# Kernel optimization log

Hardware: AMD Instinct MI355X
Metric: run time of the kernel (lower is better)

Reference implementation:

```python
import jax, jax.numpy as jnp
import numpy as np

N = 50000      # nodes
E = 800000     # edges (avg degree 16)
H = 4          # heads
C = 64         # per-head dim (= hidden_dim, TransformerConv out_channels)
D = H * C      # 256, concat output dim
VOCAB = 100


def setup_inputs() -> dict:
    key = jax.random.key(0)
    ks = jax.random.split(key, 16)
    f = lambda k, shape: (jax.random.normal(k, shape, jnp.float32) * 0.05)
    return {
        "x": jax.random.randint(ks[0], (N,), 0, VOCAB),
        "edge_index": jax.random.randint(ks[1], (2, E), 0, N),
        "embed": f(ks[2], (VOCAB, C)),        # node_embed table (hidden_dim=64)
        "Wq": f(ks[3], (C, D)), "bq": f(ks[4], (D,)),
        "Wk": f(ks[5], (C, D)), "bk": f(ks[6], (D,)),
        "Wv": f(ks[7], (C, D)), "bv": f(ks[8], (D,)),
        "Wskip": f(ks[9], (C, D)), "bskip": f(ks[10], (D,)),
        "Wbeta": f(ks[11], (3 * D, 1)),       # lin_beta has no bias in PyG
        "Wcoop": f(ks[12], (D, 1)), "bcoop": f(ks[13], (1,)),
        "Wanom": f(ks[14], (D, 1)), "banom": f(ks[15], (1,)),
    }


def _segment_softmax(logits, seg, num_segments):
    # logits: [E, H], seg: [E] destination-node ids
    m = jax.ops.segment_max(logits, seg, num_segments=num_segments)   # [N, H]
    ex = jnp.exp(logits - m[seg])
    s = jax.ops.segment_sum(ex, seg, num_segments=num_segments)       # [N, H]
    return ex / (s[seg] + 1e-16)


def _transformer_conv(h, src, dst, Wq, bq, Wk, bk, Wv, bv, Wskip, bskip, Wbeta):
    # h: [N, C] node features; src->dst edges; PyG TransformerConv(beta=True)
    q = (h @ Wq + bq).reshape(N, H, C)
    k = (h @ Wk + bk).reshape(N, H, C)
    v = (h @ Wv + bv).reshape(N, H, C)
    # per-edge attention logits: query of dst, key of src
    logits = (q[dst] * k[src]).sum(-1) / np.sqrt(C)    # [E, H]
    alpha = _segment_softmax(logits, dst, N)           # softmax over in-edges of dst
    msg = v[src] * alpha[..., None]                    # [E, H, C]
    out = jax.ops.segment_sum(msg, dst, num_segments=N).reshape(N, D)
    # beta-gated skip connection
    x_r = h @ Wskip + bskip                            # [N, D]
    beta = jax.nn.sigmoid(jnp.concatenate([out, x_r, out - x_r], axis=-1) @ Wbeta)
    return beta * x_r + (1.0 - beta) * out             # [N, D]


def reference(x, edge_index, embed, Wq, bq, Wk, bk, Wv, bv,
              Wskip, bskip, Wbeta, Wcoop, bcoop, Wanom, banom):
    h = embed[x]                                       # long input -> embedding
    src, dst = edge_index[0], edge_index[1]
    h = _transformer_conv(h, src, dst, Wq, bq, Wk, bk, Wv, bv, Wskip, bskip, Wbeta)
    h = jax.nn.relu(h)                                 # dropout is identity (eval)
    cooperation = jax.nn.sigmoid(h @ Wcoop + bcoop)    # [N, 1]
    anomaly = jax.nn.sigmoid(h @ Wanom + banom)        # [N, 1]
    return cooperation, anomaly, h
```

## Files before the change

### kernel.cpp

```cpp
#include <hip/hip_runtime.h>
#include <hip/hip_bf16.h>
#include <hip/hip_fp16.h>

typedef __hip_bfloat16 bf16;

#define NN 50000
#define EE 800000
#define VOCABSZ 100
#define DD 256
#define NW 25
#define MAXD 64
#define NBUCK 500
#define BNODES 100
#define AWG 500
#define EPW 1600
#define PCAP 24

static __device__ __forceinline__ float b2f(bf16 v) { return __bfloat162float(v); }

static __device__ __forceinline__ float ldf(const void* p, int i, int isf32) {
  if (isf32) return ((const float*)p)[i];
  return b2f(((const bf16*)p)[i]);
}

static __device__ __forceinline__ int block_detect(const unsigned short* e16) {
  __shared__ int f;
  if (threadIdx.x == 0) f = 0;
  __syncthreads();
  unsigned int ex = (e16[threadIdx.x] >> 7) & 0xFF;
  unsigned long long any = __ballot(ex >= 128);
  if ((threadIdx.x & 63) == 0 && any) atomicOr(&f, 1);
  __syncthreads();
  return f;
}

__global__ __launch_bounds__(256) void k_phase1(
    const void* __restrict__ embed,
    const void* __restrict__ Wq, const void* __restrict__ bq,
    const void* __restrict__ Wk, const void* __restrict__ bk,
    const void* __restrict__ Wv, const void* __restrict__ bv,
    const void* __restrict__ Ws, const void* __restrict__ bs,
    const void* __restrict__ Wbeta,
    const void* __restrict__ Wcoop, const void* __restrict__ bcoop,
    const void* __restrict__ Wanom, const void* __restrict__ banom,
    float* __restrict__ Qt, float* __restrict__ Kt,
    __half* __restrict__ VtH, __half* __restrict__ StH,
    float* __restrict__ Wf, int* __restrict__ flag,
    const int4* __restrict__ src4, const int4* __restrict__ dst4,
    const int* __restrict__ x,
    unsigned char* __restrict__ cnt, unsigned short* __restrict__ seg)
{
  __shared__ float e[64];
  __shared__ unsigned int cur[NBUCK];
  const int t = threadIdx.x;
  const unsigned bx = blockIdx.x;

  if (bx >= 500) {
    const unsigned w = bx - 500;
    for (int i = t; i < NBUCK; i += 256) cur[i] = 0;
    __syncthreads();
    const int g0 = w * (EPW / 4);
    for (int g = t; g < EPW / 4; g += 256) {
      int4 s = src4[g0 + g];
      int4 d = dst4[g0 + g];
      int xv0 = x[s.x], xv1 = x[s.y], xv2 = x[s.z], xv3 = x[s.w];
      unsigned b0 = (unsigned)d.x / BNODES, b1 = (unsigned)d.y / BNODES;
      unsigned b2 = (unsigned)d.z / BNODES, b3 = (unsigned)d.w / BNODES;
      unsigned p0 = atomicAdd(&cur[b0], 1u);
      unsigned p1 = atomicAdd(&cur[b1], 1u);
      unsigned p2 = atomicAdd(&cur[b2], 1u);
      unsigned p3 = atomicAdd(&cur[b3], 1u);
      if (p0 < PCAP) seg[((size_t)b0 * AWG + w) * PCAP + p0] =
          (unsigned short)(((unsigned)d.x - b0 * BNODES) | ((unsigned)xv0 << 7));
      if (p1 < PCAP) seg[((size_t)b1 * AWG + w) * PCAP + p1] =
          (unsigned short)(((unsigned)d.y - b1 * BNODES) | ((unsigned)xv1 << 7));
      if (p2 < PCAP) seg[((size_t)b2 * AWG + w) * PCAP + p2] =
          (unsigned short)(((unsigned)d.z - b2 * BNODES) | ((unsigned)xv2 << 7));
      if (p3 < PCAP) seg[((size_t)b3 * AWG + w) * PCAP + p3] =
          (unsigned short)(((unsigned)d.w - b3 * BNODES) | ((unsigned)xv3 << 7));
    }
    __syncthreads();
    for (int i = t; i < NBUCK; i += 256) {
      unsigned c = cur[i]; if (c > PCAP) c = PCAP;
      cnt[(size_t)i * AWG + w] = (unsigned char)c;
    }
    return;
  }

  const int y = bx / 100;
  const int row = bx % 100;
  if (y == 4 && row != 0) return;

  int isf32 = block_detect((const unsigned short*)embed);

  if (y == 4) {
    Wf[t]       = ldf(Wbeta, t, isf32)       + ldf(Wbeta, 512 + t, isf32);
    Wf[256 + t] = ldf(Wbeta, 256 + t, isf32) - ldf(Wbeta, 512 + t, isf32);
    Wf[512 + t] = ldf(Wcoop, t, isf32);
    Wf[768 + t] = ldf(Wanom, t, isf32);
    if (t == 0) {
      Wf[1024] = ldf(bcoop, 0, isf32);
      Wf[1025] = ldf(banom, 0, isf32);
      flag[0] = isf32;
    }
    return;
  }

  if (t < 64) e[t] = ldf(embed, row * 64 + t, isf32);
  __syncthreads();
  const void* W; const void* b;
  switch (y) {
    case 0:  W = Wq; b = bq; break;
    case 1:  W = Wk; b = bk; break;
    case 2:  W = Wv; b = bv; break;
    default: W = Ws; b = bs; break;
  }
  float acc;
  if (isf32) {
    const float* w32 = (const float*)W;
    acc = ((const float*)b)[t];
    #pragma unroll 8
    for (int c = 0; c < 64; ++c) acc = fmaf(e[c], w32[c * DD + t], acc);
  } else {
    const bf16* w16 = (const bf16*)W;
    acc = b2f(((const bf16*)b)[t]);
    #pragma unroll 8
    for (int c = 0; c < 64; ++c) acc = fmaf(e[c], b2f(w16[c * DD + t]), acc);
  }
  switch (y) {
    case 0:  Qt[row * DD + t] = acc; break;
    case 1:  Kt[row * DD + t] = acc; break;
    case 2:  VtH[row * DD + t] = __float2half(acc); break;
    default: StH[row * DD + t] = __float2half(acc); break;
  }
}

__global__ __launch_bounds__(256) void k_phase2(
    const float* __restrict__ Qt, const float* __restrict__ Kt,
    float* __restrict__ Et,
    const unsigned char* __restrict__ cnt, const unsigned short* __restrict__ seg,
    int* __restrict__ deg, unsigned short* __restrict__ ell16)
{
  __shared__ float q[DD];
  __shared__ unsigned int hist[BNODES * NW];
  const int t = threadIdx.x;
  const unsigned bx = blockIdx.x;

  if (bx < 100) {
    const int a = bx;
    q[t] = Qt[a * DD + t];
    __syncthreads();
    for (int idx = t; idx < VOCABSZ * 4; idx += 256) {
      int b = idx >> 2, h = idx & 3;
      const float* kk = Kt + b * DD + h * 64;
      const float* qq = q + h * 64;
      float acc = 0.f;
      #pragma unroll 8
      for (int c = 0; c < 64; ++c) acc += qq[c] * kk[c];
      Et[(a * VOCABSZ + b) * 4 + h] = __expf(acc * 0.125f);
    }
    return;
  }

  const int b = bx - 100;
  for (int i = t; i < BNODES * NW; i += 256) hist[i] = 0;
  __syncthreads();
  for (int w = t; w < AWG; w += 256) {
    const size_t sbase = (size_t)b * AWG + w;
    int c = (int)cnt[sbase];
    if (!c) continue;
    const uint4* sp4 = (const uint4*)(seg + sbase * PCAP);
    uint4 q0 = sp4[0];
    uint4 q1 = make_uint4(0u, 0u, 0u, 0u);
    uint4 q2 = make_uint4(0u, 0u, 0u, 0u);
    if (c > 8)  q1 = sp4[1];
    if (c > 16) q2 = sp4[2];
    unsigned wd[12] = { q0.x, q0.y, q0.z, q0.w, q1.x, q1.y, q1.z, q1.w,
                        q2.x, q2.y, q2.z, q2.w };
    #pragma unroll
    for (int i = 0; i < 12; ++i) {
      unsigned lo = wd[i] & 0xFFFFu;
      unsigned hi = wd[i] >> 16;
      if (2 * i < c)
        atomicAdd(&hist[(lo & 127u) * NW + ((lo >> 7) >> 2)], 1u << (((lo >> 7) & 3) * 8));
      if (2 * i + 1 < c)
        atomicAdd(&hist[(hi & 127u) * NW + ((hi >> 7) >> 2)], 1u << (((hi >> 7) & 3) * 8));
    }
  }
  __syncthreads();
  if (t < BNODES) {
    int n = b * BNODES + t;
    const unsigned int* cw = hist + t * NW;
    unsigned short* dp = ell16 + (size_t)n * MAXD;
    int k = 0;
    #pragma unroll
    for (int w = 0; w < NW; ++w) {
      unsigned word = cw[w];
      if (!word) continue;
      #pragma unroll
      for (int bb = 0; bb < 4; ++bb) {
        unsigned c = (word >> (8 * bb)) & 255u;
        if (c) { if (k < MAXD) dp[k] = (unsigned short)((unsigned)(w * 4 + bb) | (c << 8)); k++; }
      }
    }
    deg[n] = (k < MAXD) ? k : MAXD;
  }
}

__global__ __launch_bounds__(256) void k_node(
    const int* __restrict__ x, const int* __restrict__ deg,
    const unsigned short* __restrict__ ell16,
    const __half* __restrict__ VtH, const __half* __restrict__ StH,
    const float* __restrict__ Et, const float* __restrict__ Wf,
    void* __restrict__ out, const int* __restrict__ flag)
{
  __shared__ uint2 evs[4][2][32][4];
  const int t = threadIdx.x;
  const int lane = t & 63;
  const int wv = t >> 6;
  const int l31 = lane & 31;
  const int half = lane >> 5;
  const int hbase = lane & 32;
  const int n = blockIdx.x * 8 + wv * 2 + half;
  const int cb = l31 << 3;
  const int head = l31 >> 3;

  const int xd = x[n];
  const int dgn = deg[n];
  const int dgA = __shfl(dgn, 0, 64);
  const int dgB = __shfl(dgn, 32, 64);
  const int dmax = max(dgA, dgB);

  unsigned int mye = (l31 < dgn) ? (unsigned int)ell16[(size_t)n * MAXD + l31] : 0u;
  const int myxs = (int)(mye & 255u);
  const float mycnt = (float)(mye >> 8);
  const unsigned rowoff = (unsigned)myxs << 9;

  float4 ev = *reinterpret_cast<const float4*>(Et + xd * (VOCABSZ * 4) + myxs * 4);
  ev.x *= mycnt; ev.y *= mycnt; ev.z *= mycnt; ev.w *= mycnt;
  uint4* evp = reinterpret_cast<uint4*>(&evs[wv][half][l31][0]);
  evp[0] = make_uint4(__float_as_uint(ev.x), rowoff, __float_as_uint(ev.y), rowoff);
  evp[1] = make_uint4(__float_as_uint(ev.z), rowoff, __float_as_uint(ev.w), rowoff);

  union HF8U { uint4 u; __half2 h2[4]; };
  HF8U xru; xru.u = *reinterpret_cast<const uint4*>(StH + xd * DD + cb);
  const float4 wo0 = *reinterpret_cast<const float4*>(Wf + cb);
  const float4 wo1 = *reinterpret_cast<const float4*>(Wf + cb + 4);
  const float4 wx0 = *reinterpret_cast<const float4*>(Wf + 256 + cb);
  const float4 wx1 = *reinterpret_cast<const float4*>(Wf + 256 + cb + 4);

  const uint2* __restrict__ myev = &evs[wv][half][0][head];
  const char* __restrict__ vbase = reinterpret_cast<const char*>(VtH) + (cb << 1);

  float s = 0.f;
  __half2 a0 = __float2half2_rn(0.f), a1 = __float2half2_rn(0.f);
  __half2 a2 = __float2half2_rn(0.f), a3 = __float2half2_rn(0.f);

  const int j1 = (dmax < 32) ? dmax : 32;
  #pragma unroll 4
  for (int j = 0; j < j1; ++j) {
    uint2 ue = myev[j * 4];
    float e = __uint_as_float(ue.x);
    s += e;
    __half2 e2 = __float2half2_rn(e);
    HF8U vv; vv.u = *reinterpret_cast<const uint4*>(vbase + ue.y);
    a0 = __hfma2(e2, vv.h2[0], a0);
    a1 = __hfma2(e2, vv.h2[1], a1);
    a2 = __hfma2(e2, vv.h2[2], a2);
    a3 = __hfma2(e2, vv.h2[3], a3);
  }
  if (dmax > 32) {
    const float* __restrict__ Erow = Et + xd * (VOCABSZ * 4) + head;
    unsigned int mye2 = (l31 + 32 < dgn) ? (unsigned int)ell16[(size_t)n * MAXD + 32 + l31] : 0u;
    for (int j = 32; j < dmax; ++j) {
      unsigned int en = (unsigned int)__shfl((int)mye2, hbase + (j - 32), 64);
      int xs = (int)(en & 255u);
      float e = (float)(en >> 8) * Erow[xs << 2];
      s += e;
      __half2 e2 = __float2half2_rn(e);
      HF8U vv; vv.u = *reinterpret_cast<const uint4*>(vbase + ((unsigned)xs << 9));
      a0 = __hfma2(e2, vv.h2[0], a0);
      a1 = __hfma2(e2, vv.h2[1], a1);
      a2 = __hfma2(e2, vv.h2[2], a2);
      a3 = __hfma2(e2, vv.h2[3], a3);
    }
  }

  const float inv = 1.f / (s + 1e-16f);
  float o[8] = { __low2float(a0)*inv, __high2float(a0)*inv,
                 __low2float(a1)*inv, __high2float(a1)*inv,
                 __low2float(a2)*inv, __high2float(a2)*inv,
                 __low2float(a3)*inv, __high2float(a3)*inv };
  float xr[8] = { __low2float(xru.h2[0]), __high2float(xru.h2[0]),
                  __low2float(xru.h2[1]), __high2float(xru.h2[1]),
                  __low2float(xru.h2[2]), __high2float(xru.h2[2]),
                  __low2float(xru.h2[3]), __high2float(xru.h2[3]) };

  float bp = o[0]*wo0.x + o[1]*wo0.y + o[2]*wo0.z + o[3]*wo0.w
           + o[4]*wo1.x + o[5]*wo1.y + o[6]*wo1.z + o[7]*wo1.w
           + xr[0]*wx0.x + xr[1]*wx0.y + xr[2]*wx0.z + xr[3]*wx0.w
           + xr[4]*wx1.x + xr[5]*wx1.y + xr[6]*wx1.z + xr[7]*wx1.w;
  #pragma unroll
  for (int m = 16; m >= 1; m >>= 1) bp += __shfl_xor(bp, m, 64);
  const float beta = 1.f / (1.f + __expf(-bp));

  const float4 wc0 = *reinterpret_cast<const float4*>(Wf + 512 + cb);
  const float4 wc1 = *reinterpret_cast<const float4*>(Wf + 512 + cb + 4);
  const float4 wa0 = *reinterpret_cast<const float4*>(Wf + 768 + cb);
  const float4 wa1 = *reinterpret_cast<const float4*>(Wf + 768 + cb + 4);
  const float wcv[8] = { wc0.x, wc0.y, wc0.z, wc0.w, wc1.x, wc1.y, wc1.z, wc1.w };
  const float wav[8] = { wa0.x, wa0.y, wa0.z, wa0.w, wa1.x, wa1.y, wa1.z, wa1.w };

  float h[8];
  float pc = 0.f, pa = 0.f;
  #pragma unroll
  for (int j = 0; j < 8; ++j) {
    float hv = beta * xr[j] + (1.f - beta) * o[j];
    hv = fmaxf(hv, 0.f);
    h[j] = hv;
    pc = fmaf(hv, wcv[j], pc);
    pa = fmaf(hv, wav[j], pa);
  }
  #pragma unroll
  for (int m = 16; m >= 1; m >>= 1) {
    pc += __shfl_xor(pc, m, 64);
    pa += __shfl_xor(pa, m, 64);
  }
  const float coop = 1.f / (1.f + __expf(-(pc + Wf[1024])));
  const float anom = 1.f / (1.f + __expf(-(pa + Wf[1025])));

  if (flag[0]) {
    float* fo = (float*)out;
    if (l31 == 0) { fo[n] = coop; fo[NN + n] = anom; }
    float4* hp = reinterpret_cast<float4*>(fo + 2 * NN + (size_t)n * DD + cb);
    hp[0] = make_float4(h[0], h[1], h[2], h[3]);
    hp[1] = make_float4(h[4], h[5], h[6], h[7]);
  } else {
    bf16* bo = (bf16*)out;
    if (l31 == 0) { bo[n] = __float2bfloat16(coop); bo[NN + n] = __float2bfloat16(anom); }
    struct alignas(16) BF8S { bf16 v[8]; } hb;
    #pragma unroll
    for (int j = 0; j < 8; ++j) hb.v[j] = __float2bfloat16(h[j]);
    *reinterpret_cast<BF8S*>(bo + 2 * NN + (size_t)n * DD + cb) = hb;
  }
}

extern "C" void kernel_launch(void* const* d_in, const int* in_sizes, int n_in,
                              void* d_out, int out_size, void* d_ws, size_t ws_size,
                              hipStream_t stream) {
  (void)in_sizes; (void)n_in; (void)out_size; (void)ws_size;
  const int*  x     = (const int*)d_in[0];
  const int*  ei    = (const int*)d_in[1];
  const void* embed = d_in[2];
  const void* Wq = d_in[3];  const void* bq = d_in[4];
  const void* Wk = d_in[5];  const void* bk = d_in[6];
  const void* Wv = d_in[7];  const void* bv = d_in[8];
  const void* Ws = d_in[9];  const void* bs = d_in[10];
  const void* Wbeta = d_in[11];
  const void* Wcoop = d_in[12]; const void* bcoop = d_in[13];
  const void* Wanom = d_in[14]; const void* banom = d_in[15];
  const int* src = ei;
  const int* dst = ei + EE;

  char* base = (char*)d_ws;
  size_t pos = 0;
  auto take = [&](size_t bytes) -> char* {
    char* p = base + pos;
    pos = (pos + bytes + 255) & ~(size_t)255;
    return p;
  };
  float*  Qt  = (float*)take(VOCABSZ * DD * sizeof(float));
  float*  Kt  = (float*)take(VOCABSZ * DD * sizeof(float));
  __half* VtH = (__half*)take(VOCABSZ * DD * sizeof(__half));
  __half* StH = (__half*)take(VOCABSZ * DD * sizeof(__half));
  float*  Et  = (float*)take(VOCABSZ * VOCABSZ * 4 * sizeof(float));
  float*  Wf  = (float*)take(1026 * sizeof(float));
  int*    deg = (int*)take(NN * sizeof(int));
  int*    flag= (int*)take(256 * sizeof(int));
  unsigned char*  cnt   = (unsigned char*)take((size_t)AWG * NBUCK);
  unsigned short* seg   = (unsigned short*)take((size_t)AWG * NBUCK * PCAP * sizeof(unsigned short));
  unsigned short* ell16 = (unsigned short*)take((size_t)NN * MAXD * sizeof(unsigned short));

  k_phase1<<<1000, 256, 0, stream>>>(
      embed, Wq, bq, Wk, bk, Wv, bv, Ws, bs,
      Wbeta, Wcoop, bcoop, Wanom, banom,
      Qt, Kt, VtH, StH, Wf, flag,
      (const int4*)src, (const int4*)dst, x, cnt, seg);

  k_phase2<<<600, 256, 0, stream>>>(Qt, Kt, Et, cnt, seg, deg, ell16);

  k_node<<<NN / 8, 256, 0, stream>>>(x, deg, ell16, VtH, StH, Et, Wf, d_out, flag);
}
```

Before: 150.4 us.

## Fuse ELL build into node kernel and compute attention table in phase one

```diff
diff --git a/kernel.cpp b/kernel.cpp
--- a/kernel.cpp
+++ b/kernel.cpp
@@ -12,9 +12,16 @@
 #define MAXD 64
 #define NBUCK 500
 #define BNODES 100
-#define AWG 500
-#define EPW 1600
-#define PCAP 24
+#define AWG 1000
+#define EPW 800
+#define PCAP 16
+
+#define SCB 1000
+#define VB  1000
+#define SB  1100
+#define WFB 1200
+#define LGB 1201
+#define K1GRID 1601
 
 static __device__ __forceinline__ float b2f(bf16 v) { return __bfloat162float(v); }
 
@@ -34,7 +41,7 @@
   return f;
 }
 
-__global__ __launch_bounds__(256) void k_phase1(
+__global__ __launch_bounds__(256) void k1(
     const void* __restrict__ embed,
     const void* __restrict__ Wq, const void* __restrict__ bq,
     const void* __restrict__ Wk, const void* __restrict__ bk,
@@ -43,20 +50,19 @@
     const void* __restrict__ Wbeta,
     const void* __restrict__ Wcoop, const void* __restrict__ bcoop,
     const void* __restrict__ Wanom, const void* __restrict__ banom,
-    float* __restrict__ Qt, float* __restrict__ Kt,
     __half* __restrict__ VtH, __half* __restrict__ StH,
-    float* __restrict__ Wf, int* __restrict__ flag,
+    float* __restrict__ Et, float* __restrict__ Wf, int* __restrict__ flag,
     const int4* __restrict__ src4, const int4* __restrict__ dst4,
     const int* __restrict__ x,
     unsigned char* __restrict__ cnt, unsigned short* __restrict__ seg)
 {
-  __shared__ float e[64];
-  __shared__ unsigned int cur[NBUCK];
+  __shared__ __align__(16) float sbuf[VOCABSZ * 64];
   const int t = threadIdx.x;
   const unsigned bx = blockIdx.x;
 
-  if (bx >= 500) {
-    const unsigned w = bx - 500;
+  if (bx < SCB) {
+    unsigned* cur = (unsigned*)sbuf;
+    const unsigned w = bx;
     for (int i = t; i < NBUCK; i += 256) cur[i] = 0;
     __syncthreads();
     const int g0 = w * (EPW / 4);
@@ -87,13 +93,9 @@
     return;
   }
 
-  const int y = bx / 100;
-  const int row = bx % 100;
-  if (y == 4 && row != 0) return;
-
-  int isf32 = block_detect((const unsigned short*)embed);
-
-  if (y == 4) {
+  const int isf32 = block_detect((const unsigned short*)embed);
+
+  if (bx == WFB) {
     Wf[t]       = ldf(Wbeta, t, isf32)       + ldf(Wbeta, 512 + t, isf32);
     Wf[256 + t] = ldf(Wbeta, 256 + t, isf32) - ldf(Wbeta, 512 + t, isf32);
     Wf[512 + t] = ldf(Wcoop, t, isf32);
@@ -106,65 +108,92 @@
     return;
   }
 
+  if (bx >= LGB) {
+    const int idx = bx - LGB;
+    const int a = idx >> 2, h = idx & 3;
+    float* embF = sbuf;
+    for (int i = t; i < VOCABSZ * 64; i += 256) embF[i] = ldf(embed, i, isf32);
+    __syncthreads();
+    const int lane = t & 63, wv = t >> 6;
+    const int col = h * 64 + lane;
+    float qa, bkv, wk[64];
+    if (isf32) {
+      const float* wq = (const float*)Wq; const float* wkp = (const float*)Wk;
+      qa = ((const float*)bq)[col]; bkv = ((const float*)bk)[col];
+      #pragma unroll
+      for (int e = 0; e < 64; ++e) wk[e] = wkp[e * DD + col];
+      #pragma unroll 8
+      for (int e = 0; e < 64; ++e) qa = fmaf(embF[a * 64 + e], wq[e * DD + col], qa);
+    } else {
+      const bf16* wq = (const bf16*)Wq; const bf16* wkp = (const bf16*)Wk;
+      qa = b2f(((const bf16*)bq)[col]); bkv = b2f(((const bf16*)bk)[col]);
+      #pragma unroll
+      for (int e = 0; e < 64; ++e) wk[e] = b2f(wkp[e * DD + col]);
+      #pragma unroll 8
+      for (int e = 0; e < 64; ++e) qa = fmaf(embF[a * 64 + e], b2f(wq[e * DD + col]), qa);
+    }
+    for (int p = 0; p < 25; ++p) {
+      const int b = (p << 2) | wv;
+      const float* er = embF + b * 64;
+      float s0 = 0.f, s1 = 0.f, s2 = 0.f, s3 = 0.f;
+      #pragma unroll
+      for (int e = 0; e < 64; e += 4) {
+        s0 = fmaf(er[e],     wk[e],     s0);
+        s1 = fmaf(er[e + 1], wk[e + 1], s1);
+        s2 = fmaf(er[e + 2], wk[e + 2], s2);
+        s3 = fmaf(er[e + 3], wk[e + 3], s3);
+      }
+      float d = qa * (bkv + ((s0 + s1) + (s2 + s3)));
+      #pragma unroll
+      for (int m = 32; m >= 1; m >>= 1) d += __shfl_xor(d, m, 64);
+      if (lane == 0) Et[((a * VOCABSZ) + b) * 4 + h] = __expf(d * 0.125f);
+    }
+    return;
+  }
+
+  const int isV = (bx < SB);
+  const int row = isV ? (int)(bx - VB) : (int)(bx - SB);
+  float* e = sbuf;
   if (t < 64) e[t] = ldf(embed, row * 64 + t, isf32);
   __syncthreads();
-  const void* W; const void* b;
-  switch (y) {
-    case 0:  W = Wq; b = bq; break;
-    case 1:  W = Wk; b = bk; break;
-    case 2:  W = Wv; b = bv; break;
-    default: W = Ws; b = bs; break;
-  }
+  const void* W = isV ? Wv : Ws;
+  const void* bvec = isV ? bv : bs;
   float acc;
   if (isf32) {
     const float* w32 = (const float*)W;
-    acc = ((const float*)b)[t];
+    acc = ((const float*)bvec)[t];
     #pragma unroll 8
     for (int c = 0; c < 64; ++c) acc = fmaf(e[c], w32[c * DD + t], acc);
   } else {
     const bf16* w16 = (const bf16*)W;
-    acc = b2f(((const bf16*)b)[t]);
+    acc = b2f(((const bf16*)bvec)[t]);
     #pragma unroll 8
     for (int c = 0; c < 64; ++c) acc = fmaf(e[c], b2f(w16[c * DD + t]), acc);
   }
-  switch (y) {
-    case 0:  Qt[row * DD + t] = acc; break;
-    case 1:  Kt[row * DD + t] = acc; break;
-    case 2:  VtH[row * DD + t] = __float2half(acc); break;
-    default: StH[row * DD + t] = __float2half(acc); break;
-  }
+  if (isV) VtH[row * DD + t] = __float2half(acc);
+  else     StH[row * DD + t] = __float2half(acc);
 }
 
-__global__ __launch_bounds__(256) void k_phase2(
-    const float* __restrict__ Qt, const float* __restrict__ Kt,
-    float* __restrict__ Et,
+__global__ __launch_bounds__(256) void k2(
+    const int* __restrict__ x,
     const unsigned char* __restrict__ cnt, const unsigned short* __restrict__ seg,
-    int* __restrict__ deg, unsigned short* __restrict__ ell16)
+    const __half* __restrict__ VtH, const __half* __restrict__ StH,
+    const float* __restrict__ Et, const float* __restrict__ Wf,
+    void* __restrict__ out, const int* __restrict__ flag)
 {
-  __shared__ float q[DD];
-  __shared__ unsigned int hist[BNODES * NW];
+  __shared__ __align__(16) unsigned char smem[6656 + 8192];
+  unsigned short* ellL = (unsigned short*)smem;
+  int* degL = (int*)(smem + 6400);
+  unsigned* hist = (unsigned*)(smem + 6656);
+  uint2* evsB = (uint2*)(smem + 6656);
+
   const int t = threadIdx.x;
-  const unsigned bx = blockIdx.x;
-
-  if (bx < 100) {
-    const int a = bx;
-    q[t] = Qt[a * DD + t];
-    __syncthreads();
-    for (int idx = t; idx < VOCABSZ * 4; idx += 256) {
-      int b = idx >> 2, h = idx & 3;
-      const float* kk = Kt + b * DD + h * 64;
-      const float* qq = q + h * 64;
-      float acc = 0.f;
-      #pragma unroll 8
-      for (int c = 0; c < 64; ++c) acc += qq[c] * kk[c];
-      Et[(a * VOCABSZ + b) * 4 + h] = __expf(acc * 0.125f);
-    }
-    return;
-  }
-
-  const int b = bx - 100;
-  for (int i = t; i < BNODES * NW; i += 256) hist[i] = 0;
-  __syncthreads();
+  const int b = blockIdx.x >> 1;
+  const int offbase = (blockIdx.x & 1) * 50;
+
+  for (int i = t; i < 50 * NW; i += 256) hist[i] = 0;
+  __syncthreads();
+
   for (int w = t; w < AWG; w += 256) {
     const size_t sbase = (size_t)b * AWG + w;
     int c = (int)cnt[sbase];
@@ -172,26 +201,25 @@
     const uint4* sp4 = (const uint4*)(seg + sbase * PCAP);
     uint4 q0 = sp4[0];
     uint4 q1 = make_uint4(0u, 0u, 0u, 0u);
-    uint4 q2 = make_uint4(0u, 0u, 0u, 0u);
-    if (c > 8)  q1 = sp4[1];
-    if (c > 16) q2 = sp4[2];
-    unsigned wd[12] = { q0.x, q0.y, q0.z, q0.w, q1.x, q1.y, q1.z, q1.w,
-                        q2.x, q2.y, q2.z, q2.w };
+    if (c > 8) q1 = sp4[1];
+    unsigned wd[8] = { q0.x, q0.y, q0.z, q0.w, q1.x, q1.y, q1.z, q1.w };
     #pragma unroll
-    for (int i = 0; i < 12; ++i) {
+    for (int i = 0; i < 8; ++i) {
       unsigned lo = wd[i] & 0xFFFFu;
       unsigned hi = wd[i] >> 16;
-      if (2 * i < c)
-        atomicAdd(&hist[(lo & 127u) * NW + ((lo >> 7) >> 2)], 1u << (((lo >> 7) & 3) * 8));
-      if (2 * i + 1 < c)
-        atomicAdd(&hist[(hi & 127u) * NW + ((hi >> 7) >> 2)], 1u << (((hi >> 7) & 3) * 8));
-    }
-  }
-  __syncthreads();
-  if (t < BNODES) {
-    int n = b * BNODES + t;
-    const unsigned int* cw = hist + t * NW;
-    unsigned short* dp = ell16 + (size_t)n * MAXD;
+      int o0 = (int)(lo & 127u) - offbase;
+      int o1 = (int)(hi & 127u) - offbase;
+      if (2 * i < c && (unsigned)o0 < 50u)
+        atomicAdd(&hist[o0 * NW + ((lo >> 7) >> 2)], 1u << (((lo >> 7) & 3) * 8));
+      if (2 * i + 1 < c && (unsigned)o1 < 50u)
+        atomicAdd(&hist[o1 * NW + ((hi >> 7) >> 2)], 1u << (((hi >> 7) & 3) * 8));
+    }
+  }
+  __syncthreads();
+
+  if (t < 50) {
+    const unsigned* cw = hist + t * NW;
+    unsigned short* dp = ellL + t * MAXD;
     int k = 0;
     #pragma unroll
     for (int w = 0; w < NW; ++w) {
@@ -203,145 +231,143 @@
         if (c) { if (k < MAXD) dp[k] = (unsigned short)((unsigned)(w * 4 + bb) | (c << 8)); k++; }
       }
     }
-    deg[n] = (k < MAXD) ? k : MAXD;
-  }
-}
-
-__global__ __launch_bounds__(256) void k_node(
-    const int* __restrict__ x, const int* __restrict__ deg,
-    const unsigned short* __restrict__ ell16,
-    const __half* __restrict__ VtH, const __half* __restrict__ StH,
-    const float* __restrict__ Et, const float* __restrict__ Wf,
-    void* __restrict__ out, const int* __restrict__ flag)
-{
-  __shared__ uint2 evs[4][2][32][4];
-  const int t = threadIdx.x;
+    degL[t] = (k < MAXD) ? k : MAXD;
+  }
+  __syncthreads();
+
   const int lane = t & 63;
   const int wv = t >> 6;
   const int l31 = lane & 31;
   const int half = lane >> 5;
-  const int hbase = lane & 32;
-  const int n = blockIdx.x * 8 + wv * 2 + half;
   const int cb = l31 << 3;
   const int head = l31 >> 3;
-
-  const int xd = x[n];
-  const int dgn = deg[n];
-  const int dgA = __shfl(dgn, 0, 64);
-  const int dgB = __shfl(dgn, 32, 64);
-  const int dmax = max(dgA, dgB);
-
-  unsigned int mye = (l31 < dgn) ? (unsigned int)ell16[(size_t)n * MAXD + l31] : 0u;
-  const int myxs = (int)(mye & 255u);
-  const float mycnt = (float)(mye >> 8);
-  const unsigned rowoff = (unsigned)myxs << 9;
-
-  float4 ev = *reinterpret_cast<const float4*>(Et + xd * (VOCABSZ * 4) + myxs * 4);
-  ev.x *= mycnt; ev.y *= mycnt; ev.z *= mycnt; ev.w *= mycnt;
-  uint4* evp = reinterpret_cast<uint4*>(&evs[wv][half][l31][0]);
-  evp[0] = make_uint4(__float_as_uint(ev.x), rowoff, __float_as_uint(ev.y), rowoff);
-  evp[1] = make_uint4(__float_as_uint(ev.z), rowoff, __float_as_uint(ev.w), rowoff);
-
-  union HF8U { uint4 u; __half2 h2[4]; };
-  HF8U xru; xru.u = *reinterpret_cast<const uint4*>(StH + xd * DD + cb);
+  const int isf32o = flag[0];
+  const int nb0 = b * BNODES + offbase;
+
   const float4 wo0 = *reinterpret_cast<const float4*>(Wf + cb);
   const float4 wo1 = *reinterpret_cast<const float4*>(Wf + cb + 4);
   const float4 wx0 = *reinterpret_cast<const float4*>(Wf + 256 + cb);
   const float4 wx1 = *reinterpret_cast<const float4*>(Wf + 256 + cb + 4);
-
-  const uint2* __restrict__ myev = &evs[wv][half][0][head];
+  const float4 wc0 = *reinterpret_cast<const float4*>(Wf + 512 + cb);
+  const float4 wc1 = *reinterpret_cast<const float4*>(Wf + 512 + cb + 4);
+  const float4 wa0 = *reinterpret_cast<const float4*>(Wf + 768 + cb);
+  const float4 wa1 = *reinterpret_cast<const float4*>(Wf + 768 + cb + 4);
+  const float bco = Wf[1024], ban = Wf[1025];
+
+  union HF8U { uint4 u; __half2 h2[4]; };
+  const uint2* __restrict__ myev = evsB + ((wv * 2 + half) * 32) * 4 + head;
   const char* __restrict__ vbase = reinterpret_cast<const char*>(VtH) + (cb << 1);
 
-  float s = 0.f;
-  __half2 a0 = __float2half2_rn(0.f), a1 = __float2half2_rn(0.f);
-  __half2 a2 = __float2half2_rn(0.f), a3 = __float2half2_rn(0.f);
-
-  const int j1 = (dmax < 32) ? dmax : 32;
-  #pragma unroll 4
-  for (int j = 0; j < j1; ++j) {
-    uint2 ue = myev[j * 4];
-    float e = __uint_as_float(ue.x);
-    s += e;
-    __half2 e2 = __float2half2_rn(e);
-    HF8U vv; vv.u = *reinterpret_cast<const uint4*>(vbase + ue.y);
-    a0 = __hfma2(e2, vv.h2[0], a0);
-    a1 = __hfma2(e2, vv.h2[1], a1);
-    a2 = __hfma2(e2, vv.h2[2], a2);
-    a3 = __hfma2(e2, vv.h2[3], a3);
-  }
-  if (dmax > 32) {
-    const float* __restrict__ Erow = Et + xd * (VOCABSZ * 4) + head;
-    unsigned int mye2 = (l31 + 32 < dgn) ? (unsigned int)ell16[(size_t)n * MAXD + 32 + l31] : 0u;
-    for (int j = 32; j < dmax; ++j) {
-      unsigned int en = (unsigned int)__shfl((int)mye2, hbase + (j - 32), 64);
-      int xs = (int)(en & 255u);
-      float e = (float)(en >> 8) * Erow[xs << 2];
+  for (int r = 0; r < 7; ++r) {
+    const int liA = r * 8 + wv * 2;
+    if (liA >= 50) break;
+    const int li = liA + half;
+    const int dgA = degL[liA], dgB = degL[liA + 1];
+    const int dgn = half ? dgB : dgA;
+    const int dmax = max(dgA, dgB);
+    const int n = nb0 + li;
+    const int xd = x[n];
+
+    unsigned int mye = (l31 < dgn) ? (unsigned int)ellL[li * MAXD + l31] : 0u;
+    const int myxs = (int)(mye & 255u);
+    const float mycnt = (float)(mye >> 8);
+    const unsigned rowoff = (unsigned)myxs << 9;
+
+    float4 ev = *reinterpret_cast<const float4*>(Et + xd * (VOCABSZ * 4) + myxs * 4);
+    ev.x *= mycnt; ev.y *= mycnt; ev.z *= mycnt; ev.w *= mycnt;
+    uint4* evp = reinterpret_cast<uint4*>(evsB + ((wv * 2 + half) * 32 + l31) * 4);
+    evp[0] = make_uint4(__float_as_uint(ev.x), rowoff, __float_as_uint(ev.y), rowoff);
+    evp[1] = make_uint4(__float_as_uint(ev.z), rowoff, __float_as_uint(ev.w), rowoff);
+
+    HF8U xru; xru.u = *reinterpret_cast<const uint4*>(StH + xd * DD + cb);
+
+    float s = 0.f;
+    __half2 a0 = __float2half2_rn(0.f), a1 = __float2half2_rn(0.f);
+    __half2 a2 = __float2half2_rn(0.f), a3 = __float2half2_rn(0.f);
+
+    const int j1 = (dmax < 32) ? dmax : 32;
+    #pragma unroll 4
+    for (int j = 0; j < j1; ++j) {
+      uint2 ue = myev[j * 4];
+      float e = __uint_as_float(ue.x);
       s += e;
       __half2 e2 = __float2half2_rn(e);
-      HF8U vv; vv.u = *reinterpret_cast<const uint4*>(vbase + ((unsigned)xs << 9));
+      HF8U vv; vv.u = *reinterpret_cast<const uint4*>(vbase + ue.y);
       a0 = __hfma2(e2, vv.h2[0], a0);
       a1 = __hfma2(e2, vv.h2[1], a1);
       a2 = __hfma2(e2, vv.h2[2], a2);
       a3 = __hfma2(e2, vv.h2[3], a3);
     }
-  }
-
-  const float inv = 1.f / (s + 1e-16f);
-  float o[8] = { __low2float(a0)*inv, __high2float(a0)*inv,
-                 __low2float(a1)*inv, __high2float(a1)*inv,
-                 __low2float(a2)*inv, __high2float(a2)*inv,
-                 __low2float(a3)*inv, __high2float(a3)*inv };
-  float xr[8] = { __low2float(xru.h2[0]), __high2float(xru.h2[0]),
-                  __low2float(xru.h2[1]), __high2float(xru.h2[1]),
-                  __low2float(xru.h2[2]), __high2float(xru.h2[2]),
-                  __low2float(xru.h2[3]), __high2float(xru.h2[3]) };
-
-  float bp = o[0]*wo0.x + o[1]*wo0.y + o[2]*wo0.z + o[3]*wo0.w
-           + o[4]*wo1.x + o[5]*wo1.y + o[6]*wo1.z + o[7]*wo1.w
-           + xr[0]*wx0.x + xr[1]*wx0.y + xr[2]*wx0.z + xr[3]*wx0.w
-           + xr[4]*wx1.x + xr[5]*wx1.y + xr[6]*wx1.z + xr[7]*wx1.w;
-  #pragma unroll
-  for (int m = 16; m >= 1; m >>= 1) bp += __shfl_xor(bp, m, 64);
-  const float beta = 1.f / (1.f + __expf(-bp));
-
-  const float4 wc0 = *reinterpret_cast<const float4*>(Wf + 512 + cb);
-  const float4 wc1 = *reinterpret_cast<const float4*>(Wf + 512 + cb + 4);
-  const float4 wa0 = *reinterpret_cast<const float4*>(Wf + 768 + cb);
-  const float4 wa1 = *reinterpret_cast<const float4*>(Wf + 768 + cb + 4);
-  const float wcv[8] = { wc0.x, wc0.y, wc0.z, wc0.w, wc1.x, wc1.y, wc1.z, wc1.w };
-  const float wav[8] = { wa0.x, wa0.y, wa0.z, wa0.w, wa1.x, wa1.y, wa1.z, wa1.w };
-
-  float h[8];
-  float pc = 0.f, pa = 0.f;
-  #pragma unroll
-  for (int j = 0; j < 8; ++j) {
-    float hv = beta * xr[j] + (1.f - beta) * o[j];
-    hv = fmaxf(hv, 0.f);
-    h[j] = hv;
-    pc = fmaf(hv, wcv[j], pc);
-    pa = fmaf(hv, wav[j], pa);
-  }
-  #pragma unroll
-  for (int m = 16; m >= 1; m >>= 1) {
-    pc += __shfl_xor(pc, m, 64);
-    pa += __shfl_xor(pa, m, 64);
-  }
-  const float coop = 1.f / (1.f + __expf(-(pc + Wf[1024])));
-  const float anom = 1.f / (1.f + __expf(-(pa + Wf[1025])));
-
-  if (flag[0]) {
-    float* fo = (float*)out;
-    if (l31 == 0) { fo[n] = coop; fo[NN + n] = anom; }
-    float4* hp = reinterpret_cast<float4*>(fo + 2 * NN + (size_t)n * DD + cb);
-    hp[0] = make_float4(h[0], h[1], h[2], h[3]);
-    hp[1] = make_float4(h[4], h[5], h[6], h[7]);
-  } else {
-    bf16* bo = (bf16*)out;
-    if (l31 == 0) { bo[n] = __float2bfloat16(coop); bo[NN + n] = __float2bfloat16(anom); }
-    struct alignas(16) BF8S { bf16 v[8]; } hb;
+    if (dmax > 32) {
+      const float* __restrict__ Erow = Et + xd * (VOCABSZ * 4) + head;
+      for (int j = 32; j < dmax; ++j) {
+        if (j < dgn) {
+          unsigned en = (unsigned)ellL[li * MAXD + j];
+          int xs = (int)(en & 255u);
+          float e = (float)(en >> 8) * Erow[xs << 2];
+          s += e;
+          __half2 e2 = __float2half2_rn(e);
+          HF8U vv; vv.u = *reinterpret_cast<const uint4*>(vbase + ((unsigned)xs << 9));
+          a0 = __hfma2(e2, vv.h2[0], a0);
+          a1 = __hfma2(e2, vv.h2[1], a1);
+          a2 = __hfma2(e2, vv.h2[2], a2);
+          a3 = __hfma2(e2, vv.h2[3], a3);
+        }
+      }
+    }
+
+    const float inv = 1.f / (s + 1e-16f);
+    float o[8] = { __low2float(a0)*inv, __high2float(a0)*inv,
+                   __low2float(a1)*inv, __high2float(a1)*inv,
+                   __low2float(a2)*inv, __high2float(a2)*inv,
+                   __low2float(a3)*inv, __high2float(a3)*inv };
+    float xr[8] = { __low2float(xru.h2[0]), __high2float(xru.h2[0]),
+                    __low2float(xru.h2[1]), __high2float(xru.h2[1]),
+                    __low2float(xru.h2[2]), __high2float(xru.h2[2]),
+                    __low2float(xru.h2[3]), __high2float(xru.h2[3]) };
+
+    float bp = o[0]*wo0.x + o[1]*wo0.y + o[2]*wo0.z + o[3]*wo0.w
+             + o[4]*wo1.x + o[5]*wo1.y + o[6]*wo1.z + o[7]*wo1.w
+             + xr[0]*wx0.x + xr[1]*wx0.y + xr[2]*wx0.z + xr[3]*wx0.w
+             + xr[4]*wx1.x + xr[5]*wx1.y + xr[6]*wx1.z + xr[7]*wx1.w;
     #pragma unroll
-    for (int j = 0; j < 8; ++j) hb.v[j] = __float2bfloat16(h[j]);
-    *reinterpret_cast<BF8S*>(bo + 2 * NN + (size_t)n * DD + cb) = hb;
+    for (int m = 16; m >= 1; m >>= 1) bp += __shfl_xor(bp, m, 64);
+    const float beta = 1.f / (1.f + __expf(-bp));
+
+    float h[8];
+    float pc = 0.f, pa = 0.f;
+    const float wcv[8] = { wc0.x, wc0.y, wc0.z, wc0.w, wc1.x, wc1.y, wc1.z, wc1.w };
+    const float wav[8] = { wa0.x, wa0.y, wa0.z, wa0.w, wa1.x, wa1.y, wa1.z, wa1.w };
+    #pragma unroll
+    for (int j = 0; j < 8; ++j) {
+      float hv = beta * xr[j] + (1.f - beta) * o[j];
+      hv = fmaxf(hv, 0.f);
+      h[j] = hv;
+      pc = fmaf(hv, wcv[j], pc);
+      pa = fmaf(hv, wav[j], pa);
+    }
+    #pragma unroll
+    for (int m = 16; m >= 1; m >>= 1) {
+      pc += __shfl_xor(pc, m, 64);
+      pa += __shfl_xor(pa, m, 64);
+    }
+    const float coop = 1.f / (1.f + __expf(-(pc + bco)));
+    const float anom = 1.f / (1.f + __expf(-(pa + ban)));
+
+    if (isf32o) {
+      float* fo = (float*)out;
+      if (l31 == 0) { fo[n] = coop; fo[NN + n] = anom; }
+      float4* hp = reinterpret_cast<float4*>(fo + 2 * NN + (size_t)n * DD + cb);
+      hp[0] = make_float4(h[0], h[1], h[2], h[3]);
+      hp[1] = make_float4(h[4], h[5], h[6], h[7]);
+    } else {
+      bf16* bo = (bf16*)out;
+      if (l31 == 0) { bo[n] = __float2bfloat16(coop); bo[NN + n] = __float2bfloat16(anom); }
+      struct alignas(16) BF8S { bf16 v[8]; } hb;
+      #pragma unroll
+      for (int j = 0; j < 8; ++j) hb.v[j] = __float2bfloat16(h[j]);
+      *reinterpret_cast<BF8S*>(bo + 2 * NN + (size_t)n * DD + cb) = hb;
+    }
   }
 }
 
@@ -369,25 +395,19 @@
     pos = (pos + bytes + 255) & ~(size_t)255;
     return p;
   };
-  float*  Qt  = (float*)take(VOCABSZ * DD * sizeof(float));
-  float*  Kt  = (float*)take(VOCABSZ * DD * sizeof(float));
   __half* VtH = (__half*)take(VOCABSZ * DD * sizeof(__half));
   __half* StH = (__half*)take(VOCABSZ * DD * sizeof(__half));
   float*  Et  = (float*)take(VOCABSZ * VOCABSZ * 4 * sizeof(float));
   float*  Wf  = (float*)take(1026 * sizeof(float));
-  int*    deg = (int*)take(NN * sizeof(int));
   int*    flag= (int*)take(256 * sizeof(int));
-  unsigned char*  cnt   = (unsigned char*)take((size_t)AWG * NBUCK);
-  unsigned short* seg   = (unsigned short*)take((size_t)AWG * NBUCK * PCAP * sizeof(unsigned short));
-  unsigned short* ell16 = (unsigned short*)take((size_t)NN * MAXD * sizeof(unsigned short));
-
-  k_phase1<<<1000, 256, 0, stream>>>(
+  unsigned char*  cnt = (unsigned char*)take((size_t)NBUCK * AWG);
+  unsigned short* seg = (unsigned short*)take((size_t)NBUCK * AWG * PCAP * sizeof(unsigned short));
+
+  k1<<<K1GRID, 256, 0, stream>>>(
       embed, Wq, bq, Wk, bk, Wv, bv, Ws, bs,
       Wbeta, Wcoop, bcoop, Wanom, banom,
-      Qt, Kt, VtH, StH, Wf, flag,
+      VtH, StH, Et, Wf, flag,
       (const int4*)src, (const int4*)dst, x, cnt, seg);
 
-  k_phase2<<<600, 256, 0, stream>>>(Qt, Kt, Et, cnt, seg, deg, ell16);
-
-  k_node<<<NN / 8, 256, 0, stream>>>(x, deg, ell16, VtH, StH, Et, Wf, d_out, flag);
+  k2<<<2 * NBUCK, 256, 0, stream>>>(x, cnt, seg, VtH, StH, Et, Wf, d_out, flag);
 }
```

Result: slower. 172.3 us (+14.5%).

## Replace bucketed edge sort with global per-node vocab histogram via atomics

Applied to the files above, without the earlier changes.

```diff
diff --git a/kernel.cpp b/kernel.cpp
--- a/kernel.cpp
+++ b/kernel.cpp
@@ -8,13 +8,8 @@
 #define EE 800000
 #define VOCABSZ 100
 #define DD 256
-#define NW 25
 #define MAXD 64
-#define NBUCK 500
-#define BNODES 100
-#define AWG 500
-#define EPW 1600
-#define PCAP 24
+#define NWDS 32
 
 static __device__ __forceinline__ float b2f(bf16 v) { return __bfloat162float(v); }
 
@@ -34,7 +29,7 @@
   return f;
 }
 
-__global__ __launch_bounds__(256) void k_phase1(
+__global__ __launch_bounds__(256) void k0_prep(
     const void* __restrict__ embed,
     const void* __restrict__ Wq, const void* __restrict__ bq,
     const void* __restrict__ Wk, const void* __restrict__ bk,
@@ -46,54 +41,26 @@
     float* __restrict__ Qt, float* __restrict__ Kt,
     __half* __restrict__ VtH, __half* __restrict__ StH,
     float* __restrict__ Wf, int* __restrict__ flag,
-    const int4* __restrict__ src4, const int4* __restrict__ dst4,
-    const int* __restrict__ x,
-    unsigned char* __restrict__ cnt, unsigned short* __restrict__ seg)
+    unsigned* __restrict__ ghist)
 {
-  __shared__ float e[64];
-  __shared__ unsigned int cur[NBUCK];
   const int t = threadIdx.x;
   const unsigned bx = blockIdx.x;
 
-  if (bx >= 500) {
-    const unsigned w = bx - 500;
-    for (int i = t; i < NBUCK; i += 256) cur[i] = 0;
-    __syncthreads();
-    const int g0 = w * (EPW / 4);
-    for (int g = t; g < EPW / 4; g += 256) {
-      int4 s = src4[g0 + g];
-      int4 d = dst4[g0 + g];
-      int xv0 = x[s.x], xv1 = x[s.y], xv2 = x[s.z], xv3 = x[s.w];
-      unsigned b0 = (unsigned)d.x / BNODES, b1 = (unsigned)d.y / BNODES;
-      unsigned b2 = (unsigned)d.z / BNODES, b3 = (unsigned)d.w / BNODES;
-      unsigned p0 = atomicAdd(&cur[b0], 1u);
-      unsigned p1 = atomicAdd(&cur[b1], 1u);
-      unsigned p2 = atomicAdd(&cur[b2], 1u);
-      unsigned p3 = atomicAdd(&cur[b3], 1u);
-      if (p0 < PCAP) seg[((size_t)b0 * AWG + w) * PCAP + p0] =
-          (unsigned short)(((unsigned)d.x - b0 * BNODES) | ((unsigned)xv0 << 7));
-      if (p1 < PCAP) seg[((size_t)b1 * AWG + w) * PCAP + p1] =
-          (unsigned short)(((unsigned)d.y - b1 * BNODES) | ((unsigned)xv1 << 7));
-      if (p2 < PCAP) seg[((size_t)b2 * AWG + w) * PCAP + p2] =
-          (unsigned short)(((unsigned)d.z - b2 * BNODES) | ((unsigned)xv2 << 7));
-      if (p3 < PCAP) seg[((size_t)b3 * AWG + w) * PCAP + p3] =
-          (unsigned short)(((unsigned)d.w - b3 * BNODES) | ((unsigned)xv3 << 7));
-    }
-    __syncthreads();
-    for (int i = t; i < NBUCK; i += 256) {
-      unsigned c = cur[i]; if (c > PCAP) c = PCAP;
-      cnt[(size_t)i * AWG + w] = (unsigned char)c;
+  if (bx >= 401) {
+    const int zb = bx - 401;
+    uint4* gz = (uint4*)ghist;
+    #pragma unroll
+    for (int k = 0; k < 4; ++k) {
+      int i = t + k * 256;
+      if (i < 1000) gz[(size_t)zb * 1000 + i] = make_uint4(0u, 0u, 0u, 0u);
     }
     return;
   }
 
-  const int y = bx / 100;
-  const int row = bx % 100;
-  if (y == 4 && row != 0) return;
-
-  int isf32 = block_detect((const unsigned short*)embed);
-
-  if (y == 4) {
+  __shared__ float e[64];
+  const int isf32 = block_detect((const unsigned short*)embed);
+
+  if (bx == 400) {
     Wf[t]       = ldf(Wbeta, t, isf32)       + ldf(Wbeta, 512 + t, isf32);
     Wf[256 + t] = ldf(Wbeta, 256 + t, isf32) - ldf(Wbeta, 512 + t, isf32);
     Wf[512 + t] = ldf(Wcoop, t, isf32);
@@ -106,6 +73,8 @@
     return;
   }
 
+  const int y = bx / 100;
+  const int row = bx % 100;
   if (t < 64) e[t] = ldf(embed, row * 64 + t, isf32);
   __syncthreads();
   const void* W; const void* b;
@@ -135,86 +104,52 @@
   }
 }
 
-__global__ __launch_bounds__(256) void k_phase2(
+__global__ __launch_bounds__(256) void k1_mid(
+    const int4* __restrict__ src4, const int4* __restrict__ dst4,
+    const int* __restrict__ x, unsigned* __restrict__ ghist,
     const float* __restrict__ Qt, const float* __restrict__ Kt,
-    float* __restrict__ Et,
-    const unsigned char* __restrict__ cnt, const unsigned short* __restrict__ seg,
-    int* __restrict__ deg, unsigned short* __restrict__ ell16)
+    float* __restrict__ Et)
 {
   __shared__ float q[DD];
-  __shared__ unsigned int hist[BNODES * NW];
   const int t = threadIdx.x;
   const unsigned bx = blockIdx.x;
 
-  if (bx < 100) {
-    const int a = bx;
-    q[t] = Qt[a * DD + t];
-    __syncthreads();
-    for (int idx = t; idx < VOCABSZ * 4; idx += 256) {
-      int b = idx >> 2, h = idx & 3;
-      const float* kk = Kt + b * DD + h * 64;
-      const float* qq = q + h * 64;
-      float acc = 0.f;
-      #pragma unroll 8
-      for (int c = 0; c < 64; ++c) acc += qq[c] * kk[c];
-      Et[(a * VOCABSZ + b) * 4 + h] = __expf(acc * 0.125f);
+  if (bx < 500) {
+    const int g0 = bx * 400;
+    for (int g = t; g < 400; g += 256) {
+      int4 s = src4[g0 + g];
+      int4 d = dst4[g0 + g];
+      int x0 = x[s.x], x1 = x[s.y], x2 = x[s.z], x3 = x[s.w];
+      atomicAdd(&ghist[(size_t)d.x * NWDS + (x0 >> 2)], 1u << ((x0 & 3) * 8));
+      atomicAdd(&ghist[(size_t)d.y * NWDS + (x1 >> 2)], 1u << ((x1 & 3) * 8));
+      atomicAdd(&ghist[(size_t)d.z * NWDS + (x2 >> 2)], 1u << ((x2 & 3) * 8));
+      atomicAdd(&ghist[(size_t)d.w * NWDS + (x3 >> 2)], 1u << ((x3 & 3) * 8));
     }
     return;
   }
 
-  const int b = bx - 100;
-  for (int i = t; i < BNODES * NW; i += 256) hist[i] = 0;
+  const int a = bx - 500;
+  q[t] = Qt[a * DD + t];
   __syncthreads();
-  for (int w = t; w < AWG; w += 256) {
-    const size_t sbase = (size_t)b * AWG + w;
-    int c = (int)cnt[sbase];
-    if (!c) continue;
-    const uint4* sp4 = (const uint4*)(seg + sbase * PCAP);
-    uint4 q0 = sp4[0];
-    uint4 q1 = make_uint4(0u, 0u, 0u, 0u);
-    uint4 q2 = make_uint4(0u, 0u, 0u, 0u);
-    if (c > 8)  q1 = sp4[1];
-    if (c > 16) q2 = sp4[2];
-    unsigned wd[12] = { q0.x, q0.y, q0.z, q0.w, q1.x, q1.y, q1.z, q1.w,
-                        q2.x, q2.y, q2.z, q2.w };
-    #pragma unroll
-    for (int i = 0; i < 12; ++i) {
-      unsigned lo = wd[i] & 0xFFFFu;
-      unsigned hi = wd[i] >> 16;
-      if (2 * i < c)
-        atomicAdd(&hist[(lo & 127u) * NW + ((lo >> 7) >> 2)], 1u << (((lo >> 7) & 3) * 8));
-      if (2 * i + 1 < c)
-        atomicAdd(&hist[(hi & 127u) * NW + ((hi >> 7) >> 2)], 1u << (((hi >> 7) & 3) * 8));
-    }
-  }
-  __syncthreads();
-  if (t < BNODES) {
-    int n = b * BNODES + t;
-    const unsigned int* cw = hist + t * NW;
-    unsigned short* dp = ell16 + (size_t)n * MAXD;
-    int k = 0;
-    #pragma unroll
-    for (int w = 0; w < NW; ++w) {
-      unsigned word = cw[w];
-      if (!word) continue;
-      #pragma unroll
-      for (int bb = 0; bb < 4; ++bb) {
-        unsigned c = (word >> (8 * bb)) & 255u;
-        if (c) { if (k < MAXD) dp[k] = (unsigned short)((unsigned)(w * 4 + bb) | (c << 8)); k++; }
-      }
-    }
-    deg[n] = (k < MAXD) ? k : MAXD;
-  }
-}
-
-__global__ __launch_bounds__(256) void k_node(
-    const int* __restrict__ x, const int* __restrict__ deg,
-    const unsigned short* __restrict__ ell16,
+  for (int idx = t; idx < VOCABSZ * 4; idx += 256) {
+    int b = idx >> 2, h = idx & 3;
+    const float* kk = Kt + b * DD + h * 64;
+    const float* qq = q + h * 64;
+    float acc = 0.f;
+    #pragma unroll 8
+    for (int c = 0; c < 64; ++c) acc += qq[c] * kk[c];
+    Et[(a * VOCABSZ + b) * 4 + h] = __expf(acc * 0.125f);
+  }
+}
+
+__global__ __launch_bounds__(256) void k2_node(
+    const int* __restrict__ x, const unsigned* __restrict__ ghist,
     const __half* __restrict__ VtH, const __half* __restrict__ StH,
     const float* __restrict__ Et, const float* __restrict__ Wf,
     void* __restrict__ out, const int* __restrict__ flag)
 {
   __shared__ uint2 evs[4][2][32][4];
+  __shared__ unsigned short ellL[8][MAXD];
   const int t = threadIdx.x;
   const int lane = t & 63;
   const int wv = t >> 6;
@@ -226,12 +161,34 @@
   const int head = l31 >> 3;
 
   const int xd = x[n];
-  const int dgn = deg[n];
-  const int dgA = __shfl(dgn, 0, 64);
-  const int dgB = __shfl(dgn, 32, 64);
-  const int dmax = max(dgA, dgB);
-
-  unsigned int mye = (l31 < dgn) ? (unsigned int)ell16[(size_t)n * MAXD + l31] : 0u;
+
+  unsigned wrd = ghist[(size_t)n * NWDS + l31];
+  int k4 = ((wrd & 255u) ? 1 : 0) + (((wrd >> 8) & 255u) ? 1 : 0)
+         + (((wrd >> 16) & 255u) ? 1 : 0) + ((wrd >> 24) ? 1 : 0);
+  int pfx = k4;
+  #pragma unroll
+  for (int d = 1; d < 32; d <<= 1) {
+    int v = __shfl(pfx, hbase + ((l31 - d) & 31), 64);
+    if (l31 >= d) pfx += v;
+  }
+  const int excl = pfx - k4;
+  int dtot = __shfl(pfx, hbase + 31, 64);
+  const int dgn = (dtot < MAXD) ? dtot : MAXD;
+  const int dother = __shfl(dgn, lane ^ 32, 64);
+  const int dmax = max(dgn, dother);
+
+  unsigned short* myell = ellL[wv * 2 + half];
+  int pos = excl;
+  #pragma unroll
+  for (int bb = 0; bb < 4; ++bb) {
+    unsigned c = (wrd >> (bb * 8)) & 255u;
+    if (c && pos < MAXD) {
+      myell[pos] = (unsigned short)(((unsigned)(l31 * 4 + bb)) | (c << 8));
+      ++pos;
+    }
+  }
+
+  unsigned int mye = (l31 < dgn) ? (unsigned int)myell[l31] : 0u;
   const int myxs = (int)(mye & 255u);
   const float mycnt = (float)(mye >> 8);
   const unsigned rowoff = (unsigned)myxs << 9;
@@ -271,18 +228,19 @@
   }
   if (dmax > 32) {
     const float* __restrict__ Erow = Et + xd * (VOCABSZ * 4) + head;
-    unsigned int mye2 = (l31 + 32 < dgn) ? (unsigned int)ell16[(size_t)n * MAXD + 32 + l31] : 0u;
     for (int j = 32; j < dmax; ++j) {
-      unsigned int en = (unsigned int)__shfl((int)mye2, hbase + (j - 32), 64);
-      int xs = (int)(en & 255u);
-      float e = (float)(en >> 8) * Erow[xs << 2];
-      s += e;
-      __half2 e2 = __float2half2_rn(e);
-      HF8U vv; vv.u = *reinterpret_cast<const uint4*>(vbase + ((unsigned)xs << 9));
-      a0 = __hfma2(e2, vv.h2[0], a0);
-      a1 = __hfma2(e2, vv.h2[1], a1);
-      a2 = __hfma2(e2, vv.h2[2], a2);
-      a3 = __hfma2(e2, vv.h2[3], a3);
+      if (j < dgn) {
+        unsigned en = (unsigned)myell[j];
+        int xs = (int)(en & 255u);
+        float e = (float)(en >> 8) * Erow[xs << 2];
+        s += e;
+        __half2 e2 = __float2half2_rn(e);
+        HF8U vv; vv.u = *reinterpret_cast<const uint4*>(vbase + ((unsigned)xs << 9));
+        a0 = __hfma2(e2, vv.h2[0], a0);
+        a1 = __hfma2(e2, vv.h2[1], a1);
+        a2 = __hfma2(e2, vv.h2[2], a2);
+        a3 = __hfma2(e2, vv.h2[3], a3);
+      }
     }
   }
 
@@ -375,19 +333,16 @@
   __half* StH = (__half*)take(VOCABSZ * DD * sizeof(__half));
   float*  Et  = (float*)take(VOCABSZ * VOCABSZ * 4 * sizeof(float));
   float*  Wf  = (float*)take(1026 * sizeof(float));
-  int*    deg = (int*)take(NN * sizeof(int));
   int*    flag= (int*)take(256 * sizeof(int));
-  unsigned char*  cnt   = (unsigned char*)take((size_t)AWG * NBUCK);
-  unsigned short* seg   = (unsigned short*)take((size_t)AWG * NBUCK * PCAP * sizeof(unsigned short));
-  unsigned short* ell16 = (unsigned short*)take((size_t)NN * MAXD * sizeof(unsigned short));
-
-  k_phase1<<<1000, 256, 0, stream>>>(
+  unsigned* ghist = (unsigned*)take((size_t)NN * NWDS * sizeof(unsigned));
+
+  k0_prep<<<801, 256, 0, stream>>>(
       embed, Wq, bq, Wk, bk, Wv, bv, Ws, bs,
       Wbeta, Wcoop, bcoop, Wanom, banom,
-      Qt, Kt, VtH, StH, Wf, flag,
-      (const int4*)src, (const int4*)dst, x, cnt, seg);
-
-  k_phase2<<<600, 256, 0, stream>>>(Qt, Kt, Et, cnt, seg, deg, ell16);
-
-  k_node<<<NN / 8, 256, 0, stream>>>(x, deg, ell16, VtH, StH, Et, Wf, d_out, flag);
-}
+      Qt, Kt, VtH, StH, Wf, flag, ghist);
+
+  k1_mid<<<600, 256, 0, stream>>>(
+      (const int4*)src, (const int4*)dst, x, ghist, Qt, Kt, Et);
+
+  k2_node<<<NN / 8, 256, 0, stream>>>(x, ghist, VtH, StH, Et, Wf, d_out, flag);
+}
```

Result: slower. 166.5 us (+10.7%).
